# Kernel tuning notes

Measured on AMD Instinct MI355X. Metric: run time of the kernel, lower is better.

Reference implementation:

```python
import jax, jax.numpy as jnp
import numpy as np

B, S, D = 8, 2048, 768

def setup_inputs() -> dict:
    key = jax.random.key(0)
    k1, k2, k3, k4 = jax.random.split(key, 4)
    scale = 1.0 / np.sqrt(D)
    x = jax.random.normal(k1, (B, S, D), dtype=jnp.float32)
    W = jax.random.normal(k2, (D, D), dtype=jnp.float32) * scale
    proj_w = jax.random.normal(k3, (D, D), dtype=jnp.float32) * scale
    proj_b = jax.random.normal(k4, (D,), dtype=jnp.float32) * scale
    return {"x": x, "W": W, "proj_w": proj_w, "proj_b": proj_b}


def reference(x, W, proj_w, proj_b):
    # Wx = Linear(x) with torch convention: x @ W.T  -> [B,S,D]
    Wx = jnp.einsum('bsd,ed->bse', x, W)
    # s = Wx @ x^T  -> [B,S,S]
    s = jnp.einsum('bse,bte->bst', Wx, x)
    # mask diagonal (self) with -inf
    eye = jnp.eye(S, dtype=bool)
    s = jnp.where(eye[None, :, :], -jnp.inf, s)
    a = jax.nn.softmax(s, axis=2)
    # c = a @ x -> [B,S,D]
    c = jnp.einsum('bst,btd->bsd', a, x)
    # proj + relu, residual; dropout with p=0 is identity
    c = jax.nn.relu(jnp.einsum('bsd,ed->bse', c, proj_w) + proj_b)
    return x + c
```

## Files before the change

kernel.cpp:

```cpp
#include <hip/hip_runtime.h>
#include <hip/hip_bf16.h>

typedef _Float16 fp16_t;
typedef __attribute__((ext_vector_type(8))) _Float16 fp16x8;
typedef __attribute__((ext_vector_type(4))) _Float16 fp16x4;
typedef __attribute__((ext_vector_type(4))) float fx4;

#define GLDS(g, l)                                                              \
  __builtin_amdgcn_global_load_lds(                                             \
      (const __attribute__((address_space(1))) void*)(g),                       \
      (__attribute__((address_space(3))) void*)(l), 16, 0, 0)

enum { EPI_F32 = 0, EPI_F16 = 1, EPI_FUSE = 2, EPI_SOFT = 3 };

__device__ __forceinline__ void xcd_decode(int& bx, int& by, int& bz) {
  const int nx = gridDim.x, ny = gridDim.y;
  const int lid = (int)(blockIdx.x + nx * (blockIdx.y + ny * blockIdx.z));
  const int j = lid & 7, k = lid >> 3;
  bx = k % nx;
  const int s = j + 8 * (k / nx);
  by = s % ny;
  bz = s / ny;
}

template <int EPI>
__global__ __launch_bounds__(512) void gemm_bt(
    const fp16_t* __restrict__ A1, const fp16_t* __restrict__ B1,
    void* __restrict__ Cv, int K, int lda, int ldb, long long sA,
    long long sB, long long sC, const float* __restrict__ bias,
    const float* __restrict__ resid, float* __restrict__ m_out,
    float* __restrict__ l_out) {
  __shared__ __align__(16) fp16_t As[2][256 * 32];
  __shared__ __align__(16) fp16_t Bs[2][128 * 32];
  __shared__ float smax[(EPI == EPI_SOFT) ? 512 : 1];
  __shared__ float ssum[(EPI == EPI_SOFT) ? 512 : 1];

  const int tid  = threadIdx.x;
  const int lane = tid & 63;
  const int w    = tid >> 6;
  const int wr   = w >> 1;
  const int wc   = w & 1;

  int bx, by, bz;
  xcd_decode(bx, by, bz);
  const int N = (int)gridDim.x * 128;
  const long long tile_m = (long long)by * 256;
  const long long tile_n = (long long)bx * 128;
  const long long z = bz;
  const long long aoff = z * sA + tile_m * (long long)lda;
  const long long boff = z * sB + tile_n * (long long)ldb;

  fx4 acc[4][4];
#pragma unroll
  for (int i = 0; i < 4; i++)
#pragma unroll
    for (int j = 0; j < 4; j++) acc[i][j] = (fx4){0.f, 0.f, 0.f, 0.f};

  const int r_l = lane >> 2;
  const int c_l = ((((lane & 3) + ((r_l >> 1) & 3)) & 3) << 3);
  const int frow = lane & 15;
  const int qoff = (((lane >> 4) - ((frow >> 1) & 3)) & 3) << 3;

  const size_t sa0 = (size_t)(w * 16 + r_l) * lda + c_l;
  const size_t sa1 = (size_t)(128 + w * 16 + r_l) * lda + c_l;
  const size_t sb0 = (size_t)(w * 16 + r_l) * ldb + c_l;
  const int ld0 = (w * 16) * 32;
  const int ld1 = (128 + w * 16) * 32;

  auto stage = [&](int h, int kk) {
    const fp16_t* gah = A1 + aoff + kk;
    const fp16_t* gbh = B1 + boff + kk;
    GLDS(gah + sa0, &As[h][ld0]);
    GLDS(gah + sa1, &As[h][ld1]);
    GLDS(gbh + sb0, &Bs[h][ld0]);
  };
  auto compute = [&](int h) {
    fp16x8 afh[4], bbh[4];
#pragma unroll
    for (int mi = 0; mi < 4; mi++)
      afh[mi] = *(const fp16x8*)&As[h][(wr * 64 + mi * 16 + frow) * 32 + qoff];
#pragma unroll
    for (int ni = 0; ni < 4; ni++)
      bbh[ni] = *(const fp16x8*)&Bs[h][(wc * 64 + ni * 16 + frow) * 32 + qoff];
#pragma unroll
    for (int mi = 0; mi < 4; mi++)
#pragma unroll
      for (int ni = 0; ni < 4; ni++)
        acc[mi][ni] = __builtin_amdgcn_mfma_f32_16x16x32_f16(
            afh[mi], bbh[ni], acc[mi][ni], 0, 0, 0);
  };

  for (int kt = 0; kt < K; kt += 64) {
    __syncthreads();
    stage(0, kt);
    stage(1, kt + 32);
    __syncthreads();
    compute(0);
    compute(1);
  }

  const int er = (lane >> 4) * 4;
  const int ec = lane & 15;
  const long long crow = tile_m + wr * 64;
  const long long ccol = tile_n + wc * 64;

  if constexpr (EPI == EPI_SOFT) {
#pragma unroll
    for (int mi = 0; mi < 4; mi++)
#pragma unroll
      for (int j = 0; j < 4; j++) {
        const long long r = crow + mi * 16 + er + j;
        float mx = -1e30f;
#pragma unroll
        for (int ni = 0; ni < 4; ni++) {
          const long long cc = ccol + ni * 16 + ec;
          float v = acc[mi][ni][j];
          if (r == cc) v = -1e30f;
          acc[mi][ni][j] = v;
          mx = fmaxf(mx, v);
        }
#pragma unroll
        for (int o = 1; o < 16; o <<= 1) mx = fmaxf(mx, __shfl_xor(mx, o, 64));
        if (ec == 0) smax[wc * 256 + wr * 64 + mi * 16 + er + j] = mx;
      }
    __syncthreads();
#pragma unroll
    for (int mi = 0; mi < 4; mi++)
#pragma unroll
      for (int j = 0; j < 4; j++) {
        const int rid = wr * 64 + mi * 16 + er + j;
        const float m = fmaxf(smax[rid], smax[256 + rid]);
        const long long r = crow + mi * 16 + er + j;
        float s = 0.f;
#pragma unroll
        for (int ni = 0; ni < 4; ni++) {
          const float e = __expf(acc[mi][ni][j] - m);
          s += e;
          ((fp16_t*)Cv)[z * sC + r * N + (ccol + ni * 16 + ec)] = (fp16_t)e;
        }
#pragma unroll
        for (int o = 1; o < 16; o <<= 1) s += __shfl_xor(s, o, 64);
        if (ec == 0) ssum[wc * 256 + rid] = s;
      }
    __syncthreads();
    if (tid < 256) {
      const long long si = (z * 16 + bx) * 2048 + tile_m + tid;
      m_out[si] = fmaxf(smax[tid], smax[256 + tid]);
      l_out[si] = ssum[tid] + ssum[256 + tid];
    }
  } else {
#pragma unroll
    for (int mi = 0; mi < 4; mi++)
#pragma unroll
      for (int j = 0; j < 4; j++) {
        const long long r = crow + mi * 16 + er + j;
#pragma unroll
        for (int ni = 0; ni < 4; ni++) {
          const long long cc = ccol + ni * 16 + ec;
          const long long idx = z * sC + r * N + cc;
          const float v = acc[mi][ni][j];
          if (EPI == EPI_F32) {
            ((float*)Cv)[idx] = v;
          } else if (EPI == EPI_F16) {
            ((fp16_t*)Cv)[idx] = (fp16_t)v;
          } else {
            float u = v + bias[cc];
            u = u > 0.f ? u : 0.f;
            ((float*)Cv)[idx] = resid[r * N + cc] + u;
          }
        }
      }
  }
}

__global__ __launch_bounds__(512) void gemm_pv(
    const fp16_t* __restrict__ P, const float* __restrict__ mstat,
    const float* __restrict__ lstat, const fp16_t* __restrict__ Bx,
    fp16_t* __restrict__ C) {
  __shared__ __align__(16) fp16_t As[2][256 * 32];
  __shared__ __align__(16) fp16_t Bs[2][128 * 32];
  __shared__ float sc[16][256];

  const int tid  = threadIdx.x;
  const int lane = tid & 63;
  const int w    = tid >> 6;
  const int wr   = w >> 1;
  const int wc   = w & 1;

  int bx, by, bz;
  xcd_decode(bx, by, bz);
  const long long tile_m = (long long)by * 256;
  const long long tile_n = (long long)bx * 128;
  const long long z = bz;

  if (tid < 256) {
    const long long base = z * 16 * 2048 + tile_m + tid;
    float mv[16];
    float m = -1e30f;
#pragma unroll
    for (int t = 0; t < 16; t++) {
      mv[t] = mstat[base + t * 2048];
      m = fmaxf(m, mv[t]);
    }
    float l = 0.f;
#pragma unroll
    for (int t = 0; t < 16; t++) l += lstat[base + t * 2048] * __expf(mv[t] - m);
    const float il = 1.0f / l;
#pragma unroll
    for (int t = 0; t < 16; t++) sc[t][tid] = __expf(mv[t] - m) * il;
  }

  fx4 acc[4][4];
#pragma unroll
  for (int i = 0; i < 4; i++)
#pragma unroll
    for (int j = 0; j < 4; j++) acc[i][j] = (fx4){0.f, 0.f, 0.f, 0.f};

  const int r_l = lane >> 2;
  const int c_l = ((((lane & 3) + ((r_l >> 1) & 3)) & 3) << 3);
  const int frow = lane & 15;
  const int qoff = (((lane >> 4) - ((frow >> 1) & 3)) & 3) << 3;
  const size_t s0 = (size_t)(w * 16 + r_l) * 2048 + c_l;
  const size_t s1 = (size_t)(128 + w * 16 + r_l) * 2048 + c_l;
  const int ld0 = (w * 16) * 32;
  const int ld1 = (128 + w * 16) * 32;

  const fp16_t* A = P + z * (2048LL * 2048) + tile_m * 2048;
  const fp16_t* B = Bx + z * (768LL * 2048) + tile_n * 2048;

  auto stage = [&](int h, int kk) {
    GLDS(A + kk + s0, &As[h][ld0]);
    GLDS(A + kk + s1, &As[h][ld1]);
    GLDS(B + kk + s0, &Bs[h][ld0]);
  };
  auto compute = [&](int h, const fp16_t* sh) {
    fp16x8 af[4], bb[4];
#pragma unroll
    for (int mi = 0; mi < 4; mi++) {
      af[mi] = *(const fp16x8*)&As[h][(wr * 64 + mi * 16 + frow) * 32 + qoff];
      af[mi] *= sh[mi];
    }
#pragma unroll
    for (int ni = 0; ni < 4; ni++)
      bb[ni] = *(const fp16x8*)&Bs[h][(wc * 64 + ni * 16 + frow) * 32 + qoff];
#pragma unroll
    for (int mi = 0; mi < 4; mi++)
#pragma unroll
      for (int ni = 0; ni < 4; ni++)
        acc[mi][ni] = __builtin_amdgcn_mfma_f32_16x16x32_f16(
            af[mi], bb[ni], acc[mi][ni], 0, 0, 0);
  };

  for (int kt = 0; kt < 2048; kt += 64) {
    __syncthreads();
    stage(0, kt);
    stage(1, kt + 32);
    __syncthreads();
    fp16_t sh[4];
    {
      const int tt = kt >> 7;
#pragma unroll
      for (int mi = 0; mi < 4; mi++)
        sh[mi] = (fp16_t)sc[tt][wr * 64 + mi * 16 + frow];
    }
    compute(0, sh);
    compute(1, sh);
  }

  const int er = (lane >> 4) * 4;
  const int ec = lane & 15;
  const long long crow = tile_m + wr * 64;
  const long long ccol = tile_n + wc * 64;
  fp16_t* Cz = C + z * (2048LL * 768);
#pragma unroll
  for (int mi = 0; mi < 4; mi++)
#pragma unroll
    for (int j = 0; j < 4; j++) {
      const long long rr = crow + mi * 16 + er + j;
#pragma unroll
      for (int ni = 0; ni < 4; ni++)
        Cz[rr * 768 + ccol + ni * 16 + ec] = (fp16_t)acc[mi][ni][j];
    }
}

__global__ __launch_bounds__(256) void prep_x(
    const float* __restrict__ x, fp16_t* __restrict__ xhl,
    fp16_t* __restrict__ xT) {
  __shared__ fp16_t t[32][33];
  const int b = blockIdx.z;
  const int d0 = blockIdx.x * 32;
  const int s0 = blockIdx.y * 32;
  const float* ib = x + (long long)b * 2048 * 768;
  const int tx = threadIdx.x & 31;
  const int ty = threadIdx.x >> 5;
#pragma unroll
  for (int i = 0; i < 4; i++) {
    const int srow = s0 + ty + i * 8;
    const float v = ib[(long long)srow * 768 + d0 + tx];
    const fp16_t h = (fp16_t)v;
    const long long rbase = ((long long)b * 2048 + srow) * 1536;
    xhl[rbase + d0 + tx] = h;
    xhl[rbase + 768 + d0 + tx] = (fp16_t)(v - (float)h);
    t[ty + i * 8][tx] = h;
  }
  __syncthreads();
#pragma unroll
  for (int i = 0; i < 4; i++)
    xT[(long long)b * 768 * 2048 + (long long)(d0 + ty + i * 8) * 2048 + s0 + tx] =
        t[tx][ty + i * 8];
}

__global__ __launch_bounds__(256) void cast_w(
    const float* __restrict__ W, const float* __restrict__ pw,
    fp16_t* __restrict__ Whh, fp16_t* __restrict__ ph, int n4) {
  const int i = blockIdx.x * 256 + threadIdx.x;
  if (i >= n4) return;
  if (blockIdx.y == 0) {
    const float4 v = ((const float4*)W)[i];
    const fp16x4 h = {(fp16_t)v.x, (fp16_t)v.y, (fp16_t)v.z, (fp16_t)v.w};
    const int e = i * 4;
    const long long o = (long long)(e / 768) * 1536 + (e % 768);
    *(fp16x4*)&Whh[o] = h;
    *(fp16x4*)&Whh[o + 768] = h;
  } else {
    const float4 v = ((const float4*)pw)[i];
    ((fp16x4*)ph)[i] =
        (fp16x4){(fp16_t)v.x, (fp16_t)v.y, (fp16_t)v.z, (fp16_t)v.w};
  }
}

extern "C" void kernel_launch(void* const* d_in, const int* in_sizes, int n_in,
                              void* d_out, int out_size, void* d_ws,
                              size_t ws_size, hipStream_t stream) {
  const float* x  = (const float*)d_in[0];
  const float* W  = (const float*)d_in[1];
  const float* pw = (const float*)d_in[2];
  const float* pb = (const float*)d_in[3];

  const long long S = 2048, D = 768;
  const long long BS = 8 * S;

  char* p = (char*)d_ws;
  auto carve = [&](long long bytes) {
    char* q = p;
    p += (bytes + 255) & ~255LL;
    return q;
  };
  fp16_t* xhl = (fp16_t*)carve(BS * 1536 * 2);
  fp16_t* xT = (fp16_t*)carve(BS * D * 2);
  fp16_t* Wx = (fp16_t*)carve(BS * D * 2);
  fp16_t* Whh = (fp16_t*)carve(D * 1536 * 2);
  fp16_t* ph = (fp16_t*)carve(D * D * 2);
  float*  mstat = (float*)carve(BS * 16 * 4);
  float*  lstat = (float*)carve(BS * 16 * 4);
  fp16_t* Ps = (fp16_t*)carve(8 * S * S * 2);
  fp16_t* cb = Wx;

  prep_x<<<dim3(24, 64, 8), 256, 0, stream>>>(x, xhl, xT);
  cast_w<<<dim3((unsigned)(D * D / 4 / 256), 2), 256, 0, stream>>>(
      W, pw, Whh, ph, (int)(D * D / 4));

  gemm_bt<EPI_F16><<<dim3(6, 64, 1), 512, 0, stream>>>(
      xhl, Whh, Wx, 1536, 1536, 1536, 0, 0, 0, nullptr, nullptr, nullptr,
      nullptr);

  gemm_bt<EPI_SOFT><<<dim3(16, 8, 8), 512, 0, stream>>>(
      Wx, xhl, Ps, 768, 768, 1536, S * D, S * 1536, S * S, nullptr, nullptr,
      mstat, lstat);

  gemm_pv<<<dim3(6, 8, 8), 512, 0, stream>>>(Ps, mstat, lstat, xT, cb);

  gemm_bt<EPI_FUSE><<<dim3(6, 64, 1), 512, 0, stream>>>(
      cb, ph, (float*)d_out, 768, 768, 768, 0, 0, 0, pb, x, nullptr,
      nullptr);
}
```

Measured before the change: 335.9 us.

## Triple-buffer LDS with async prefetch two stages ahead in GEMM kernels

Replaces the load-all-then-compute loop, which had two barriers per 64-wide k step, with a three-buffer ring in both GEMM kernels. Each 32-wide k stage is issued two steps ahead through global_load_lds, and a vmcnt wait plus a single barrier per step lets copies overlap MFMA work. The PV kernel also keeps its softmax scale table in fp16 rather than fp32 and adds the barrier that was missing after filling it. In exchange, LDS use grows by half, which may lower occupancy. Correctness depends on the hand-set vmcnt count matching the three loads issued per stage.

```diff
diff --git a/kernel.cpp b/kernel.cpp
--- a/kernel.cpp
+++ b/kernel.cpp
@@ -30,8 +30,8 @@
     long long sB, long long sC, const float* __restrict__ bias,
     const float* __restrict__ resid, float* __restrict__ m_out,
     float* __restrict__ l_out) {
-  __shared__ __align__(16) fp16_t As[2][256 * 32];
-  __shared__ __align__(16) fp16_t Bs[2][128 * 32];
+  __shared__ __align__(16) fp16_t As[3][256 * 32];
+  __shared__ __align__(16) fp16_t Bs[3][128 * 32];
   __shared__ float smax[(EPI == EPI_SOFT) ? 512 : 1];
   __shared__ float ssum[(EPI == EPI_SOFT) ? 512 : 1];
 
@@ -67,21 +67,21 @@
   const int ld0 = (w * 16) * 32;
   const int ld1 = (128 + w * 16) * 32;
 
-  auto stage = [&](int h, int kk) {
+  auto stage = [&](int b, int kk) {
     const fp16_t* gah = A1 + aoff + kk;
     const fp16_t* gbh = B1 + boff + kk;
-    GLDS(gah + sa0, &As[h][ld0]);
-    GLDS(gah + sa1, &As[h][ld1]);
-    GLDS(gbh + sb0, &Bs[h][ld0]);
-  };
-  auto compute = [&](int h) {
+    GLDS(gah + sa0, &As[b][ld0]);
+    GLDS(gah + sa1, &As[b][ld1]);
+    GLDS(gbh + sb0, &Bs[b][ld0]);
+  };
+  auto compute = [&](int b) {
     fp16x8 afh[4], bbh[4];
 #pragma unroll
     for (int mi = 0; mi < 4; mi++)
-      afh[mi] = *(const fp16x8*)&As[h][(wr * 64 + mi * 16 + frow) * 32 + qoff];
+      afh[mi] = *(const fp16x8*)&As[b][(wr * 64 + mi * 16 + frow) * 32 + qoff];
 #pragma unroll
     for (int ni = 0; ni < 4; ni++)
-      bbh[ni] = *(const fp16x8*)&Bs[h][(wc * 64 + ni * 16 + frow) * 32 + qoff];
+      bbh[ni] = *(const fp16x8*)&Bs[b][(wc * 64 + ni * 16 + frow) * 32 + qoff];
 #pragma unroll
     for (int mi = 0; mi < 4; mi++)
 #pragma unroll
@@ -90,13 +90,22 @@
             afh[mi], bbh[ni], acc[mi][ni], 0, 0, 0);
   };
 
-  for (int kt = 0; kt < K; kt += 64) {
-    __syncthreads();
-    stage(0, kt);
-    stage(1, kt + 32);
-    __syncthreads();
-    compute(0);
-    compute(1);
+  const int NS = K >> 5;
+  stage(0, 0);
+  stage(1, 32);
+  int bsel = 0;
+  for (int s = 0; s < NS; s++) {
+    if (s + 1 < NS) asm volatile("s_waitcnt vmcnt(3)" ::: "memory");
+    else            asm volatile("s_waitcnt vmcnt(0)" ::: "memory");
+    __builtin_amdgcn_s_barrier();
+    __builtin_amdgcn_sched_barrier(0);
+    if (s + 2 < NS) {
+      int bn = bsel + 2;
+      if (bn >= 3) bn -= 3;
+      stage(bn, (s + 2) << 5);
+    }
+    compute(bsel);
+    bsel = (bsel + 1 == 3) ? 0 : bsel + 1;
   }
 
   const int er = (lane >> 4) * 4;
@@ -177,9 +186,9 @@
     const fp16_t* __restrict__ P, const float* __restrict__ mstat,
     const float* __restrict__ lstat, const fp16_t* __restrict__ Bx,
     fp16_t* __restrict__ C) {
-  __shared__ __align__(16) fp16_t As[2][256 * 32];
-  __shared__ __align__(16) fp16_t Bs[2][128 * 32];
-  __shared__ float sc[16][256];
+  __shared__ __align__(16) fp16_t As[3][256 * 32];
+  __shared__ __align__(16) fp16_t Bs[3][128 * 32];
+  __shared__ fp16_t sch[16][256];
 
   const int tid  = threadIdx.x;
   const int lane = tid & 63;
@@ -207,8 +216,10 @@
     for (int t = 0; t < 16; t++) l += lstat[base + t * 2048] * __expf(mv[t] - m);
     const float il = 1.0f / l;
 #pragma unroll
-    for (int t = 0; t < 16; t++) sc[t][tid] = __expf(mv[t] - m) * il;
-  }
+    for (int t = 0; t < 16; t++)
+      sch[t][tid] = (fp16_t)(__expf(mv[t] - m) * il);
+  }
+  __syncthreads();
 
   fx4 acc[4][4];
 #pragma unroll
@@ -228,21 +239,21 @@
   const fp16_t* A = P + z * (2048LL * 2048) + tile_m * 2048;
   const fp16_t* B = Bx + z * (768LL * 2048) + tile_n * 2048;
 
-  auto stage = [&](int h, int kk) {
-    GLDS(A + kk + s0, &As[h][ld0]);
-    GLDS(A + kk + s1, &As[h][ld1]);
-    GLDS(B + kk + s0, &Bs[h][ld0]);
-  };
-  auto compute = [&](int h, const fp16_t* sh) {
+  auto stage = [&](int b, int kk) {
+    GLDS(A + kk + s0, &As[b][ld0]);
+    GLDS(A + kk + s1, &As[b][ld1]);
+    GLDS(B + kk + s0, &Bs[b][ld0]);
+  };
+  auto compute = [&](int b, const fp16_t* sh) {
     fp16x8 af[4], bb[4];
 #pragma unroll
     for (int mi = 0; mi < 4; mi++) {
-      af[mi] = *(const fp16x8*)&As[h][(wr * 64 + mi * 16 + frow) * 32 + qoff];
+      af[mi] = *(const fp16x8*)&As[b][(wr * 64 + mi * 16 + frow) * 32 + qoff];
       af[mi] *= sh[mi];
     }
 #pragma unroll
     for (int ni = 0; ni < 4; ni++)
-      bb[ni] = *(const fp16x8*)&Bs[h][(wc * 64 + ni * 16 + frow) * 32 + qoff];
+      bb[ni] = *(const fp16x8*)&Bs[b][(wc * 64 + ni * 16 + frow) * 32 + qoff];
 #pragma unroll
     for (int mi = 0; mi < 4; mi++)
 #pragma unroll
@@ -251,20 +262,29 @@
             af[mi], bb[ni], acc[mi][ni], 0, 0, 0);
   };
 
-  for (int kt = 0; kt < 2048; kt += 64) {
-    __syncthreads();
-    stage(0, kt);
-    stage(1, kt + 32);
-    __syncthreads();
+  const int NS = 64;
+  stage(0, 0);
+  stage(1, 32);
+  int bsel = 0;
+  for (int s = 0; s < NS; s++) {
+    if (s + 1 < NS) asm volatile("s_waitcnt vmcnt(3)" ::: "memory");
+    else            asm volatile("s_waitcnt vmcnt(0)" ::: "memory");
+    __builtin_amdgcn_s_barrier();
+    __builtin_amdgcn_sched_barrier(0);
+    if (s + 2 < NS) {
+      int bn = bsel + 2;
+      if (bn >= 3) bn -= 3;
+      stage(bn, (s + 2) << 5);
+    }
     fp16_t sh[4];
     {
-      const int tt = kt >> 7;
+      const int tt = s >> 2;
 #pragma unroll
       for (int mi = 0; mi < 4; mi++)
-        sh[mi] = (fp16_t)sc[tt][wr * 64 + mi * 16 + frow];
-    }
-    compute(0, sh);
-    compute(1, sh);
+        sh[mi] = sch[tt][wr * 64 + mi * 16 + frow];
+    }
+    compute(bsel, sh);
+    bsel = (bsel + 1 == 3) ? 0 : bsel + 1;
   }
 
   const int er = (lane >> 4) * 4;
```

Measured after the change: 358.8 us. +6.8%, slower.

## Double-buffer GEMM K-loop with async LDS prefetch of the next stage

Applied to the files above, without the earlier changes.

Both GEMM kernels change from loading two K-halves and then computing with full syncs to a software pipeline. The next 32-wide K slice is issued into the alternate LDS buffer while the current one is computed, using vmcnt waits and raw barriers. The aim is to hide global-to-LDS load latency behind the MFMA work. It adds twice as many barriers per K element, depends on the exact count of outstanding loads being right for vmcnt(3), and adds an explicit sync after the softmax-scale setup.

```diff
diff --git a/kernel.cpp b/kernel.cpp
--- a/kernel.cpp
+++ b/kernel.cpp
@@ -90,13 +90,18 @@
             afh[mi], bbh[ni], acc[mi][ni], 0, 0, 0);
   };
 
-  for (int kt = 0; kt < K; kt += 64) {
-    __syncthreads();
-    stage(0, kt);
-    stage(1, kt + 32);
-    __syncthreads();
-    compute(0);
-    compute(1);
+  const int NS = K >> 5;
+  stage(0, 0);
+  for (int s = 0; s < NS; s++) {
+    if (s + 1 < NS) {
+      stage((s + 1) & 1, (s + 1) << 5);
+      asm volatile("s_waitcnt vmcnt(3)" ::: "memory");
+    } else {
+      asm volatile("s_waitcnt vmcnt(0)" ::: "memory");
+    }
+    __builtin_amdgcn_s_barrier();
+    compute(s & 1);
+    __builtin_amdgcn_s_barrier();
   }
 
   const int er = (lane >> 4) * 4;
@@ -209,6 +214,7 @@
 #pragma unroll
     for (int t = 0; t < 16; t++) sc[t][tid] = __expf(mv[t] - m) * il;
   }
+  __syncthreads();
 
   fx4 acc[4][4];
 #pragma unroll
@@ -251,20 +257,25 @@
             af[mi], bb[ni], acc[mi][ni], 0, 0, 0);
   };
 
-  for (int kt = 0; kt < 2048; kt += 64) {
-    __syncthreads();
-    stage(0, kt);
-    stage(1, kt + 32);
-    __syncthreads();
+  const int NS = 64;
+  stage(0, 0);
+  for (int s = 0; s < NS; s++) {
+    if (s + 1 < NS) {
+      stage((s + 1) & 1, (s + 1) << 5);
+      asm volatile("s_waitcnt vmcnt(3)" ::: "memory");
+    } else {
+      asm volatile("s_waitcnt vmcnt(0)" ::: "memory");
+    }
+    __builtin_amdgcn_s_barrier();
     fp16_t sh[4];
     {
-      const int tt = kt >> 7;
+      const int tt = s >> 2;
 #pragma unroll
       for (int mi = 0; mi < 4; mi++)
         sh[mi] = (fp16_t)sc[tt][wr * 64 + mi * 16 + frow];
     }
-    compute(0, sh);
-    compute(1, sh);
+    compute(s & 1, sh);
+    __builtin_amdgcn_s_barrier();
   }
 
   const int er = (lane >> 4) * 4;
```

Measured after the change: 346.4 us. 1.03x slower.
